# Kernel tuning notes

Measured on AMD Instinct MI355X. Metric: run time of the kernel, lower is better.

## Reference

```python
import jax, jax.numpy as jnp
import numpy as np
from jax import lax

SELECTION_SIZE = 2  # top-k experts per token


def setup_inputs() -> dict:
    key = jax.random.key(0)
    k1, k2, k3, k4 = jax.random.split(key, 4)
    N, E, IN, OUT = 8192, 8, 2048, 2048
    X = jax.random.normal(k1, (N, IN), dtype=jnp.float32)
    G = jax.random.normal(k2, (N, E), dtype=jnp.float32)
    # expert Linear params: y = x @ W_e.T + b_e, W_e: [out, in]
    W = jax.random.normal(k3, (E, OUT, IN), dtype=jnp.float32) * (1.0 / np.sqrt(IN))
    b = jax.random.normal(k4, (E, OUT), dtype=jnp.float32) * 0.01
    return {"X": X, "G": G, "W": W, "b": b}


def reference(X, G, W, b):
    # softmax gating over experts, then top-k selection and renormalization
    raw_weights = jax.nn.softmax(G, axis=1)                      # [N, E]
    top_w, top_idx = lax.top_k(raw_weights, SELECTION_SIZE)      # [N, k]
    norm_w = top_w / jnp.sum(top_w, axis=1, keepdims=True)       # [N, k]

    # dense all-expert GEMM (same math as per-expert gathered matmuls)
    all_Y = jnp.einsum('ni,eoi->neo', X, W) + b[None, :, :]      # [N, E, out]

    # gather the top-k experts' outputs per token and combine
    sel_Y = jnp.take_along_axis(all_Y, top_idx[:, :, None], axis=1)  # [N, k, out]
    Y = jnp.einsum('nk,nko->no', norm_w, sel_Y)                  # [N, out]
    return Y
```

## Files before the change

kernel.cpp:

```cpp
#include <hip/hip_runtime.h>
#include <hip/hip_bf16.h>

#define N_TOK 8192
#define N_EXP 8
#define DIM_IN 2048
#define DIM_OUT 2048

#define BM 256
#define BN 256
#define BK 64
#define NKT (DIM_IN / BK)

#define NX_ELEMS (N_TOK * DIM_IN)
#define NW_ELEMS (N_EXP * DIM_OUT * DIM_IN)

typedef __attribute__((ext_vector_type(8))) short bf16x8_t;
typedef __attribute__((ext_vector_type(8))) short s16x8_t;
typedef __attribute__((ext_vector_type(4))) short s16x4_t;
typedef __attribute__((ext_vector_type(4))) float f32x4_t;

__device__ __forceinline__ short f2bf(float f) {
    union { __hip_bfloat16 h; short s; } u;
    u.h = __float2bfloat16(f);
    return u.s;
}

__device__ __forceinline__ float bf2f(unsigned short s) {
    union { float f; unsigned u; } v;
    v.u = ((unsigned)s) << 16;
    return v.f;
}

__device__ __forceinline__ void gload_lds16(const void* g, void* l) {
    __builtin_amdgcn_global_load_lds(
        (const __attribute__((address_space(1))) void*)g,
        (__attribute__((address_space(3))) void*)l, 16, 0, 0);
}

__global__ void moe_zero_kernel(float4* __restrict__ y, int n4, int* __restrict__ counts) {
    int i = blockIdx.x * blockDim.x + threadIdx.x;
    if (i < N_EXP) counts[i] = 0;
    float4 z; z.x = 0.f; z.y = 0.f; z.z = 0.f; z.w = 0.f;
    for (; i < n4; i += gridDim.x * blockDim.x) y[i] = z;
}

__global__ void moe_cvt_kernel(const float* __restrict__ X, const float* __restrict__ W,
                               unsigned short* __restrict__ Xb, unsigned short* __restrict__ Wb,
                               const int* __restrict__ counts, int* __restrict__ base) {
    if (blockIdx.x == 0 && threadIdx.x == 0) {
        int s = 0;
#pragma unroll
        for (int e = 0; e < N_EXP; ++e) { base[e] = s; s += counts[e]; }
        base[N_EXP] = s;
    }
    const long long total8 = (long long)(NX_ELEMS + NW_ELEMS) / 8;
    for (long long i = blockIdx.x * blockDim.x + threadIdx.x; i < total8;
         i += (long long)gridDim.x * blockDim.x) {
        long long b8 = i * 8;
        const float* src;
        unsigned short* dst;
        if (b8 < NX_ELEMS) { src = X + b8; dst = Xb + b8; }
        else { src = W + (b8 - NX_ELEMS); dst = Wb + (b8 - NX_ELEMS); }
        f32x4_t a = __builtin_nontemporal_load((const f32x4_t*)src);
        f32x4_t b = __builtin_nontemporal_load((const f32x4_t*)(src + 4));
        s16x8_t h;
        h[0] = f2bf(a[0]); h[1] = f2bf(a[1]); h[2] = f2bf(a[2]); h[3] = f2bf(a[3]);
        h[4] = f2bf(b[0]); h[5] = f2bf(b[1]); h[6] = f2bf(b[2]); h[7] = f2bf(b[3]);
        *(s16x8_t*)dst = h;
    }
}

__global__ void moe_gate_kernel(const float* __restrict__ G,
                                int* __restrict__ counts,
                                int* __restrict__ lists,
                                float* __restrict__ lw,
                                int* __restrict__ slotA, int* __restrict__ slotB,
                                float* __restrict__ wAo, float* __restrict__ wBo) {
    int t = blockIdx.x * blockDim.x + threadIdx.x;
    if (t >= N_TOK) return;
    float g[N_EXP];
#pragma unroll
    for (int e = 0; e < N_EXP; ++e) g[e] = G[t * N_EXP + e];
    int i0 = 0; float b0 = g[0];
#pragma unroll
    for (int e = 1; e < N_EXP; ++e) if (g[e] > b0) { b0 = g[e]; i0 = e; }
    int i1 = -1; float b1 = -INFINITY;
#pragma unroll
    for (int e = 0; e < N_EXP; ++e) if (e != i0 && g[e] > b1) { b1 = g[e]; i1 = e; }
    float e1 = expf(b1 - b0);
    float w0 = 1.0f / (1.0f + e1);
    float w1 = e1 * w0;
    int p0 = atomicAdd(&counts[i0], 1);
    lists[i0 * N_TOK + p0] = t;
    lw[i0 * N_TOK + p0] = w0;
    int p1 = atomicAdd(&counts[i1], 1);
    lists[i1 * N_TOK + p1] = t;
    lw[i1 * N_TOK + p1] = w1;
    slotA[t] = (i0 << 13) | p0;
    slotB[t] = (i1 << 13) | p1;
    wAo[t] = w0;
    wBo[t] = w1;
}

__global__ __launch_bounds__(256) void moe_combine_kernel(
        const unsigned short* __restrict__ scratch, const int* __restrict__ base,
        const int* __restrict__ slotA, const int* __restrict__ slotB,
        const float* __restrict__ wA, const float* __restrict__ wB,
        float* __restrict__ Y) {
    const int t = blockIdx.x;
    const int c = threadIdx.x * 8;
    const int sa = slotA[t];
    const int sb = slotB[t];
    const long gA = base[sa >> 13] + (sa & 8191);
    const long gB = base[sb >> 13] + (sb & 8191);
    const float wa = wA[t], wb = wB[t];
    s16x8_t a = __builtin_nontemporal_load((const s16x8_t*)(scratch + gA * DIM_OUT + c));
    s16x8_t b = __builtin_nontemporal_load((const s16x8_t*)(scratch + gB * DIM_OUT + c));
    f32x4_t y0, y1;
#pragma unroll
    for (int j = 0; j < 4; ++j) {
        y0[j] = wa * bf2f((unsigned short)a[j])     + wb * bf2f((unsigned short)b[j]);
        y1[j] = wa * bf2f((unsigned short)a[j + 4]) + wb * bf2f((unsigned short)b[j + 4]);
    }
    f32x4_t* y = (f32x4_t*)(Y + (long)t * DIM_OUT + c);
    y[0] = y0;
    y[1] = y1;
}

__global__ __launch_bounds__(512, 2) void moe_gemm_bf16(
        const unsigned short* __restrict__ Xb, const unsigned short* __restrict__ Wb,
        const float* __restrict__ bias,
        const int* __restrict__ counts, const int* __restrict__ lists,
        const float* __restrict__ lw, const int* __restrict__ base,
        unsigned short* __restrict__ scratch, float* __restrict__ Y) {
    const int L = blockIdx.x + (DIM_OUT / BN) * (blockIdx.y + (N_TOK / BM) * blockIdx.z);
    const int e = L & 7;
    const int idx = L >> 3;
    const int M = counts[e];
    const int m0 = (idx >> 3) * BM;
    if (m0 >= M) return;
    int vr = M - m0; if (vr > BM) vr = BM;
    const int col0 = (idx & 7) * BN;

    __shared__ unsigned short As[2][BM * BK];
    __shared__ unsigned short Bs[2][BN * BK];

    const int tid = threadIdx.x;
    const int lane = tid & 63;
    const int wid = tid >> 6;
    const int wn = (wid & 3) * 64;

    const int* mylist = lists + e * N_TOK + m0;
    const float* lwp = lw + e * N_TOK + m0;

    const int srow = tid >> 3;
    const int scol = ((tid & 7) ^ (srow & 7)) * 8;

    const unsigned short* bptr = Wb + ((size_t)e * DIM_OUT + col0 + srow) * DIM_IN + scol;

    const int ldsbase = wid * 512;

    const int rl = lane & 15;
    const int hi = lane >> 4;
    const char* AsC = (const char*)As;
    const char* BsC = (const char*)Bs;

#define STAGE_B_H(buf, h, koff)                                                 \
    do {                                                                        \
        _Pragma("unroll")                                                       \
        for (int i = 2 * (h); i < 2 * (h) + 2; ++i)                             \
            gload_lds16(bptr + (size_t)(i * 64) * DIM_IN + (koff),              \
                        &Bs[buf][i * 4096 + ldsbase]);                          \
    } while (0)

    if (vr > 128) {
        const int wm = (wid >> 2) * 128;

        const unsigned short* aptr[4];
#pragma unroll
        for (int i = 0; i < 4; ++i) {
            int r = srow + 64 * i;
            int tok = (m0 + r < M) ? mylist[r] : mylist[0];
            aptr[i] = Xb + (size_t)tok * DIM_IN + scol;
        }

        unsigned vA[2], vB[2];
#pragma unroll
        for (int kk = 0; kk < 2; ++kk) {
            unsigned x = (unsigned)(((kk << 6) | (hi << 4)) ^ ((rl & 7) << 4));
            vA[kk] = (unsigned)((wm + rl) * 128) + x;
            vB[kk] = (unsigned)((wn + rl) * 128) + x;
        }

        f32x4_t acc[8][4];
#pragma unroll
        for (int m = 0; m < 8; ++m)
#pragma unroll
            for (int n = 0; n < 4; ++n)
                acc[m][n] = (f32x4_t)(0.0f);

#define STAGE_A_H(buf, h, koff)                                                 \
    do {                                                                        \
        _Pragma("unroll")                                                       \
        for (int i = 2 * (h); i < 2 * (h) + 2; ++i)                             \
            gload_lds16(aptr[i] + (koff), &As[buf][i * 4096 + ldsbase]);        \
    } while (0)

        STAGE_A_H(0, 0, 0);  STAGE_A_H(0, 1, 0);  STAGE_B_H(0, 0, 0);  STAGE_B_H(0, 1, 0);
        STAGE_A_H(1, 0, BK); STAGE_A_H(1, 1, BK); STAGE_B_H(1, 0, BK);

#define DO_TILE(CC, KOFN, KOF2)                                                 \
    {                                                                           \
        asm volatile("s_waitcnt vmcnt(6)" ::: "memory");                        \
        __builtin_amdgcn_s_barrier();                                           \
        asm volatile("" ::: "memory");                                          \
        STAGE_B_H(1 - (CC), 1, (KOFN));                                         \
        bf16x8_t bfr[4][2], af0[4][2], af1[4][2];                               \
        _Pragma("unroll")                                                       \
        for (int n = 0; n < 4; ++n)                                             \
            _Pragma("unroll")                                                   \
            for (int kk = 0; kk < 2; ++kk)                                      \
                bfr[n][kk] = *(const bf16x8_t*)(BsC + vB[kk] + ((CC) * 32768 + n * 2048)); \
        _Pragma("unroll")                                                       \
        for (int m = 0; m < 4; ++m)                                             \
            _Pragma("unroll")                                                   \
            for (int kk = 0; kk < 2; ++kk)                                      \
                af0[m][kk] = *(const bf16x8_t*)(AsC + vA[kk] + ((CC) * 32768 + m * 2048)); \
        __builtin_amdgcn_s_setprio(1);                                          \
        _Pragma("unroll")                                                       \
        for (int m = 0; m < 2; ++m)                                             \
            _Pragma("unroll")                                                   \
            for (int n = 0; n < 4; ++n)                                         \
                _Pragma("unroll")                                               \
                for (int kk = 0; kk < 2; ++kk)                                  \
                    acc[m][n] = __builtin_amdgcn_mfma_f32_16x16x32_bf16(af0[m][kk], bfr[n][kk], acc[m][n], 0, 0, 0); \
        __builtin_amdgcn_s_setprio(0);                                          \
        _Pragma("unroll")                                                       \
        for (int m = 0; m < 4; ++m)                                             \
            _Pragma("unroll")                                                   \
            for (int kk = 0; kk < 2; ++kk)                                      \
                af1[m][kk] = *(const bf16x8_t*)(AsC + vA[kk] + ((CC) * 32768 + (m + 4) * 2048)); \
        __builtin_amdgcn_s_setprio(1);                                          \
        _Pragma("unroll")                                                       \
        for (int m = 2; m < 4; ++m)                                             \
            _Pragma("unroll")                                                   \
            for (int n = 0; n < 4; ++n)                                         \
                _Pragma("unroll")                                               \
                for (int kk = 0; kk < 2; ++kk)                                  \
                    acc[m][n] = __builtin_amdgcn_mfma_f32_16x16x32_bf16(af0[m][kk], bfr[n][kk], acc[m][n], 0, 0, 0); \
        __builtin_amdgcn_s_setprio(0);                                          \
        asm volatile("s_waitcnt lgkmcnt(0)" ::: "memory");                      \
        __builtin_amdgcn_sched_barrier(0);                                      \
        __builtin_amdgcn_s_barrier();                                           \
        asm volatile("" ::: "memory");                                          \
        STAGE_A_H((CC), 0, (KOF2));                                             \
        __builtin_amdgcn_s_setprio(1);                                          \
        _Pragma("unroll")                                                       \
        for (int m = 0; m < 2; ++m)                                             \
            _Pragma("unroll")                                                   \
            for (int n = 0; n < 4; ++n)                                         \
                _Pragma("unroll")                                               \
                for (int kk = 0; kk < 2; ++kk)                                  \
                    acc[m + 4][n] = __builtin_amdgcn_mfma_f32_16x16x32_bf16(af1[m][kk], bfr[n][kk], acc[m + 4][n], 0, 0, 0); \
        __builtin_amdgcn_s_setprio(0);                                          \
        STAGE_A_H((CC), 1, (KOF2));                                             \
        __builtin_amdgcn_s_setprio(1);                                          \
        _Pragma("unroll")                                                       \
        for (int n = 0; n < 4; ++n)                                             \
            _Pragma("unroll")                                                   \
            for (int kk = 0; kk < 2; ++kk)                                      \
                acc[6][n] = __builtin_amdgcn_mfma_f32_16x16x32_bf16(af1[2][kk], bfr[n][kk], acc[6][n], 0, 0, 0); \
        __builtin_amdgcn_s_setprio(0);                                          \
        STAGE_B_H((CC), 0, (KOF2));                                             \
        __builtin_amdgcn_s_setprio(1);                                          \
        _Pragma("unroll")                                                       \
        for (int n = 0; n < 4; ++n)                                             \
            _Pragma("unroll")                                                   \
            for (int kk = 0; kk < 2; ++kk)                                      \
                acc[7][n] = __builtin_amdgcn_mfma_f32_16x16x32_bf16(af1[3][kk], bfr[n][kk], acc[7][n], 0, 0, 0); \
        __builtin_amdgcn_s_setprio(0);                                          \
    }

        for (int kt = 0; kt < NKT; kt += 2) {
            const int kofn0 = (kt + 1) * BK;
            const int kof20 = ((kt + 2 < NKT) ? (kt + 2) : (NKT - 1)) * BK;
            const int kofn1 = kof20;
            const int kof21 = ((kt + 3 < NKT) ? (kt + 3) : (NKT - 1)) * BK;
            DO_TILE(0, kofn0, kof20)
            DO_TILE(1, kofn1, kof21)
        }
        asm volatile("s_waitcnt vmcnt(0)" ::: "memory");

        const int cl = lane & 15;
        const int rq = (lane >> 4) << 2;
        float biasv[4];
#pragma unroll
        for (int n = 0; n < 4; ++n) biasv[n] = bias[e * DIM_OUT + col0 + wn + n * 16 + cl];

        if (scratch) {
            const int segbase = base[e] + m0;
#pragma unroll
            for (int m = 0; m < 8; ++m) {
#pragma unroll
                for (int j = 0; j < 4; ++j) {
                    int row = wm + (m << 4) + rq + j;
                    if (m0 + row < M) {
                        short* out = (short*)(scratch + (size_t)(segbase + row) * DIM_OUT + col0 + wn);
#pragma unroll
                        for (int n = 0; n < 4; ++n)
                            __builtin_nontemporal_store(f2bf(acc[m][n][j] + biasv[n]), out + n * 16 + cl);
                    }
                }
            }
        } else {
#pragma unroll
            for (int m = 0; m < 8; ++m) {
#pragma unroll
                for (int j = 0; j < 4; ++j) {
                    int row = wm + (m << 4) + rq + j;
                    if (m0 + row < M) {
                        int tok = mylist[row];
                        float wgt = lwp[row];
                        float* yrow = Y + (size_t)tok * DIM_OUT + col0 + wn;
#pragma unroll
                        for (int n = 0; n < 4; ++n)
                            atomicAdd(yrow + n * 16 + cl, wgt * (acc[m][n][j] + biasv[n]));
                    }
                }
            }
        }
    } else {
        const int wm = (wid >> 2) * 64;

        const unsigned short* aptrT[2];
#pragma unroll
        for (int i = 0; i < 2; ++i) {
            int r = srow + 64 * i;
            int tok = (m0 + r < M) ? mylist[r] : mylist[0];
            aptrT[i] = Xb + (size_t)tok * DIM_IN + scol;
        }

        unsigned vA[2], vB[2];
#pragma unroll
        for (int kk = 0; kk < 2; ++kk) {
            unsigned x = (unsigned)(((kk << 6) | (hi << 4)) ^ ((rl & 7) << 4));
            vA[kk] = (unsigned)((wm + rl) * 128) + x;
            vB[kk] = (unsigned)((wn + rl) * 128) + x;
        }

        f32x4_t acc[4][4];
#pragma unroll
        for (int m = 0; m < 4; ++m)
#pragma unroll
            for (int n = 0; n < 4; ++n)
                acc[m][n] = (f32x4_t)(0.0f);

#define STAGE_A_T(buf, koff)                                                    \
    do {                                                                        \
        _Pragma("unroll")                                                       \
        for (int i = 0; i < 2; ++i)                                             \
            gload_lds16(aptrT[i] + (koff), &As[buf][i * 4096 + ldsbase]);       \
    } while (0)

        STAGE_A_T(0, 0);  STAGE_B_H(0, 0, 0);  STAGE_B_H(0, 1, 0);
        STAGE_A_T(1, BK); STAGE_B_H(1, 0, BK);

#define DO_TILE_T(CC, KOFN, KOF2)                                               \
    {                                                                           \
        asm volatile("s_waitcnt vmcnt(4)" ::: "memory");                        \
        __builtin_amdgcn_s_barrier();                                           \
        asm volatile("" ::: "memory");                                          \
        STAGE_B_H(1 - (CC), 1, (KOFN));                                         \
        bf16x8_t bfr[4][2], af[4][2];                                           \
        _Pragma("unroll")                                                       \
        for (int n = 0; n < 4; ++n)                                             \
            _Pragma("unroll")                                                   \
            for (int kk = 0; kk < 2; ++kk)                                      \
                bfr[n][kk] = *(const bf16x8_t*)(BsC + vB[kk] + ((CC) * 32768 + n * 2048)); \
        _Pragma("unroll")                                                       \
        for (int m = 0; m < 4; ++m)                                             \
            _Pragma("unroll")                                                   \
            for (int kk = 0; kk < 2; ++kk)                                      \
                af[m][kk] = *(const bf16x8_t*)(AsC + vA[kk] + ((CC) * 32768 + m * 2048)); \
        __builtin_amdgcn_s_setprio(1);                                          \
        _Pragma("unroll")                                                       \
        for (int m = 0; m < 2; ++m)                                             \
            _Pragma("unroll")                                                   \
            for (int n = 0; n < 4; ++n)                                         \
                _Pragma("unroll")                                               \
                for (int kk = 0; kk < 2; ++kk)                                  \
                    acc[m][n] = __builtin_amdgcn_mfma_f32_16x16x32_bf16(af[m][kk], bfr[n][kk], acc[m][n], 0, 0, 0); \
        __builtin_amdgcn_s_setprio(0);                                          \
        asm volatile("s_waitcnt lgkmcnt(0)" ::: "memory");                      \
        __builtin_amdgcn_sched_barrier(0);                                      \
        __builtin_amdgcn_s_barrier();                                           \
        asm volatile("" ::: "memory");                                          \
        STAGE_A_T((CC), (KOF2));                                                \
        __builtin_amdgcn_s_setprio(1);                                          \
        _Pragma("unroll")                                                       \
        for (int m = 2; m < 4; ++m)                                             \
            _Pragma("unroll")                                                   \
            for (int n = 0; n < 4; ++n)                                         \
                _Pragma("unroll")                                               \
                for (int kk = 0; kk < 2; ++kk)                                  \
                    acc[m][n] = __builtin_amdgcn_mfma_f32_16x16x32_bf16(af[m][kk], bfr[n][kk], acc[m][n], 0, 0, 0); \
        __builtin_amdgcn_s_setprio(0);                                          \
        STAGE_B_H((CC), 0, (KOF2));                                             \
    }

        for (int kt = 0; kt < NKT; kt += 2) {
            const int kofn0 = (kt + 1) * BK;
            const int kof20 = ((kt + 2 < NKT) ? (kt + 2) : (NKT - 1)) * BK;
            const int kofn1 = kof20;
            const int kof21 = ((kt + 3 < NKT) ? (kt + 3) : (NKT - 1)) * BK;
            DO_TILE_T(0, kofn0, kof20)
            DO_TILE_T(1, kofn1, kof21)
        }
        asm volatile("s_waitcnt vmcnt(0)" ::: "memory");

        const int cl = lane & 15;
        const int rq = (lane >> 4) << 2;
        float biasv[4];
#pragma unroll
        for (int n = 0; n < 4; ++n) biasv[n] = bias[e * DIM_OUT + col0 + wn + n * 16 + cl];

        if (scratch) {
            const int segbase = base[e] + m0;
#pragma unroll
            for (int m = 0; m < 4; ++m) {
#pragma unroll
                for (int j = 0; j < 4; ++j) {
                    int row = wm + (m << 4) + rq + j;
                    if (m0 + row < M) {
                        short* out = (short*)(scratch + (size_t)(segbase + row) * DIM_OUT + col0 + wn);
#pragma unroll
                        for (int n = 0; n < 4; ++n)
                            __builtin_nontemporal_store(f2bf(acc[m][n][j] + biasv[n]), out + n * 16 + cl);
                    }
                }
            }
        } else {
#pragma unroll
            for (int m = 0; m < 4; ++m) {
#pragma unroll
                for (int j = 0; j < 4; ++j) {
                    int row = wm + (m << 4) + rq + j;
                    if (m0 + row < M) {
                        int tok = mylist[row];
                        float wgt = lwp[row];
                        float* yrow = Y + (size_t)tok * DIM_OUT + col0 + wn;
#pragma unroll
                        for (int n = 0; n < 4; ++n)
                            atomicAdd(yrow + n * 16 + cl, wgt * (acc[m][n][j] + biasv[n]));
                    }
                }
            }
        }
    }
#undef DO_TILE
#undef DO_TILE_T
#undef STAGE_A_H
#undef STAGE_A_T
#undef STAGE_B_H
}

__global__ __launch_bounds__(256, 2) void moe_gemm_f32(
        const float* __restrict__ X, const float* __restrict__ W,
        const float* __restrict__ bias,
        const int* __restrict__ counts, const int* __restrict__ lists,
        const float* __restrict__ lw, float* __restrict__ Y) {
    const int e = blockIdx.z;
    const int M = counts[e];
    const int m0 = blockIdx.y * 128;
    if (m0 >= M) return;
    const int col0 = blockIdx.x * 128;

    __shared__ short As[128 * 64];
    __shared__ short Bs[128 * 64];
    char* Ab = (char*)As;
    char* Bb = (char*)Bs;

    const int tid = threadIdx.x;
    const int lane = tid & 63;
    const int wid = tid >> 6;
    const int wm = (wid >> 1) * 64;
    const int wn = (wid & 1) * 64;

    const int* mylist = lists + e * N_TOK + m0;
    const float* lwp = lw + e * N_TOK + m0;

    const int srow = tid >> 4;
    const int scol = (tid & 15) << 2;
    const int swzW = (srow & 7) << 4;

    const float* xptr[8];
#pragma unroll
    for (int p = 0; p < 8; ++p) {
        int r = p * 16 + srow;
        int tok = (m0 + r < M) ? mylist[r] : mylist[0];
        xptr[p] = X + (size_t)tok * DIM_IN + scol;
    }
    const float* wptr = W + ((size_t)e * DIM_OUT + col0 + srow) * DIM_IN + scol;

    f32x4_t acc[4][4];
#pragma unroll
    for (int m = 0; m < 4; ++m)
#pragma unroll
        for (int n = 0; n < 4; ++n)
            acc[m][n] = (f32x4_t)(0.0f);

    for (int k0 = 0; k0 < DIM_IN; k0 += 64) {
#pragma unroll
        for (int p = 0; p < 8; ++p) {
            int r = p * 16 + srow;
            unsigned byteoff = (unsigned)(r * 128 + scol * 2) ^ swzW;
            float4 va = *(const float4*)(xptr[p] + k0);
            s16x4_t ha; ha[0] = f2bf(va.x); ha[1] = f2bf(va.y); ha[2] = f2bf(va.z); ha[3] = f2bf(va.w);
            *(s16x4_t*)(Ab + byteoff) = ha;
            float4 vb = *(const float4*)(wptr + (size_t)p * 16 * DIM_IN + k0);
            s16x4_t hb; hb[0] = f2bf(vb.x); hb[1] = f2bf(vb.y); hb[2] = f2bf(vb.z); hb[3] = f2bf(vb.w);
            *(s16x4_t*)(Bb + byteoff) = hb;
        }
        __syncthreads();

#pragma unroll
        for (int kk = 0; kk < 2; ++kk) {
            const int kb = (kk << 6) + ((lane >> 4) << 4);
            bf16x8_t af[4], bfr[4];
#pragma unroll
            for (int m = 0; m < 4; ++m) {
                int r = wm + (m << 4) + (lane & 15);
                unsigned byteoff = (unsigned)(r * 128 + kb) ^ ((unsigned)(r & 7) << 4);
                af[m] = *(const bf16x8_t*)(Ab + byteoff);
            }
#pragma unroll
            for (int n = 0; n < 4; ++n) {
                int r = wn + (n << 4) + (lane & 15);
                unsigned byteoff = (unsigned)(r * 128 + kb) ^ ((unsigned)(r & 7) << 4);
                bfr[n] = *(const bf16x8_t*)(Bb + byteoff);
            }
#pragma unroll
            for (int m = 0; m < 4; ++m)
#pragma unroll
                for (int n = 0; n < 4; ++n)
                    acc[m][n] = __builtin_amdgcn_mfma_f32_16x16x32_bf16(af[m], bfr[n], acc[m][n], 0, 0, 0);
        }
        __syncthreads();
    }

    const int cl = lane & 15;
    const int rq = (lane >> 4) << 2;
    float biasv[4];
#pragma unroll
    for (int n = 0; n < 4; ++n) biasv[n] = bias[e * DIM_OUT + col0 + wn + n * 16 + cl];
#pragma unroll
    for (int m = 0; m < 4; ++m) {
#pragma unroll
        for (int j = 0; j < 4; ++j) {
            int row = wm + (m << 4) + rq + j;
            if (m0 + row < M) {
                int tok = mylist[row];
                float wgt = lwp[row];
                float* yrow = Y + (size_t)tok * DIM_OUT + col0 + wn;
#pragma unroll
                for (int n = 0; n < 4; ++n)
                    atomicAdd(yrow + n * 16 + cl, wgt * (acc[m][n][j] + biasv[n]));
            }
        }
    }
}

extern "C" void kernel_launch(void* const* d_in, const int* in_sizes, int n_in,
                              void* d_out, int out_size, void* d_ws, size_t ws_size,
                              hipStream_t stream) {
    const float* X = (const float*)d_in[0];
    const float* G = (const float*)d_in[1];
    const float* W = (const float*)d_in[2];
    const float* b = (const float*)d_in[3];
    float* Y = (float*)d_out;

    char* ws = (char*)d_ws;
    int*   counts = (int*)ws;
    int*   base   = (int*)(ws + 64);
    int*   slotA  = (int*)(ws + 256);
    int*   slotB  = (int*)(ws + 256 + 32768);
    float* wA     = (float*)(ws + 256 + 65536);
    float* wB     = (float*)(ws + 256 + 98304);
    int*   lists  = (int*)(ws + 256 + 131072);
    float* lw     = (float*)(ws + 256 + 131072 + 262144);
    size_t o_Xb   = 256 + 131072 + 2 * 262144;
    unsigned short* Xb = (unsigned short*)(ws + o_Xb);
    size_t o_Wb   = o_Xb + (size_t)NX_ELEMS * 2;
    unsigned short* Wb = (unsigned short*)(ws + o_Wb);
    size_t o_scr  = o_Wb + (size_t)NW_ELEMS * 2;
    unsigned short* scratch = (unsigned short*)(ws + o_scr);
    const size_t ws_need_mid  = o_scr;
    const size_t ws_need_full = o_scr + (size_t)2 * N_TOK * DIM_OUT * 2;

    const bool use_scratch = (ws_size >= ws_need_full);
    const bool use_bf16    = (ws_size >= ws_need_mid);

    if (use_scratch) {
        moe_zero_kernel<<<1, 256, 0, stream>>>((float4*)Y, 0, counts);
    } else {
        moe_zero_kernel<<<2048, 256, 0, stream>>>((float4*)Y, out_size / 4, counts);
    }
    moe_gate_kernel<<<(N_TOK + 255) / 256, 256, 0, stream>>>(G, counts, lists, lw,
                                                             slotA, slotB, wA, wB);

    if (use_bf16) {
        moe_cvt_kernel<<<2048, 256, 0, stream>>>(X, W, Xb, Wb, counts, base);
        dim3 grid(DIM_OUT / BN, N_TOK / BM, N_EXP);
        moe_gemm_bf16<<<grid, 512, 0, stream>>>(Xb, Wb, b, counts, lists, lw, base,
                                                use_scratch ? scratch : nullptr, Y);
        if (use_scratch) {
            moe_combine_kernel<<<N_TOK, 256, 0, stream>>>(scratch, base, slotA, slotB,
                                                          wA, wB, Y);
        }
    } else {
        dim3 grid(DIM_OUT / 128, N_TOK / 128, N_EXP);
        moe_gemm_f32<<<grid, 256, 0, stream>>>(X, W, b, counts, lists, lw, Y);
    }
}
```

Baseline: 297.1 us.

## Restructure K-tile loop into four barrier-separated quadrant phases interleaving loads and MFMAs

Reorganizes each K-tile iteration into four phases (rows 0-3 × cols 0-1, rows 0-3 × cols 2-3, rows 4-7 × cols 0-1, rows 4-7 × cols 2-3). Each phase loads a partial set of LDS fragments, issues a slice of global->LDS prefetch, syncs with barriers, then runs MFMAs. The vmcnt wait and barrier move to the end of the tile, with one hoisted before the loop. The goal is a finer ping-pong schedule that overlaps LDS reads and global prefetch with MFMA work, at the cost of more barriers per tile. Correctness depends on the reordered buffer-overwrite timing still being safe.

```diff
diff --git a/kernel.cpp b/kernel.cpp
--- a/kernel.cpp
+++ b/kernel.cpp
@@ -208,16 +208,16 @@
 
         STAGE_A_H(0, 0, 0);  STAGE_A_H(0, 1, 0);  STAGE_B_H(0, 0, 0);  STAGE_B_H(0, 1, 0);
         STAGE_A_H(1, 0, BK); STAGE_A_H(1, 1, BK); STAGE_B_H(1, 0, BK);
+        asm volatile("s_waitcnt vmcnt(6)" ::: "memory");
+        __builtin_amdgcn_s_barrier();
+        asm volatile("" ::: "memory");
 
 #define DO_TILE(CC, KOFN, KOF2)                                                 \
     {                                                                           \
-        asm volatile("s_waitcnt vmcnt(6)" ::: "memory");                        \
-        __builtin_amdgcn_s_barrier();                                           \
-        asm volatile("" ::: "memory");                                          \
-        STAGE_B_H(1 - (CC), 1, (KOFN));                                         \
-        bf16x8_t bfr[4][2], af0[4][2], af1[4][2];                               \
-        _Pragma("unroll")                                                       \
-        for (int n = 0; n < 4; ++n)                                             \
+        bf16x8_t bfr[4][2], af03[4][2], af47[4][2];                             \
+         \
+        _Pragma("unroll")                                                       \
+        for (int n = 0; n < 2; ++n)                                             \
             _Pragma("unroll")                                                   \
             for (int kk = 0; kk < 2; ++kk)                                      \
                 bfr[n][kk] = *(const bf16x8_t*)(BsC + vB[kk] + ((CC) * 32768 + n * 2048)); \
@@ -225,60 +225,81 @@
         for (int m = 0; m < 4; ++m)                                             \
             _Pragma("unroll")                                                   \
             for (int kk = 0; kk < 2; ++kk)                                      \
-                af0[m][kk] = *(const bf16x8_t*)(AsC + vA[kk] + ((CC) * 32768 + m * 2048)); \
+                af03[m][kk] = *(const bf16x8_t*)(AsC + vA[kk] + ((CC) * 32768 + m * 2048)); \
+        STAGE_B_H(1 - (CC), 1, (KOFN));                                         \
+        __builtin_amdgcn_s_barrier();                                           \
+        asm volatile("" ::: "memory");                                          \
+        asm volatile("s_waitcnt lgkmcnt(0)" ::: "memory");                      \
+        __builtin_amdgcn_sched_barrier(0);                                      \
         __builtin_amdgcn_s_setprio(1);                                          \
         _Pragma("unroll")                                                       \
-        for (int m = 0; m < 2; ++m)                                             \
-            _Pragma("unroll")                                                   \
-            for (int n = 0; n < 4; ++n)                                         \
+        for (int m = 0; m < 4; ++m)                                             \
+            _Pragma("unroll")                                                   \
+            for (int n = 0; n < 2; ++n)                                         \
                 _Pragma("unroll")                                               \
                 for (int kk = 0; kk < 2; ++kk)                                  \
-                    acc[m][n] = __builtin_amdgcn_mfma_f32_16x16x32_bf16(af0[m][kk], bfr[n][kk], acc[m][n], 0, 0, 0); \
+                    acc[m][n] = __builtin_amdgcn_mfma_f32_16x16x32_bf16(af03[m][kk], bfr[n][kk], acc[m][n], 0, 0, 0); \
         __builtin_amdgcn_s_setprio(0);                                          \
+        __builtin_amdgcn_s_barrier();                                           \
+        asm volatile("" ::: "memory");                                          \
+                                  \
+        _Pragma("unroll")                                                       \
+        for (int n = 2; n < 4; ++n)                                             \
+            _Pragma("unroll")                                                   \
+            for (int kk = 0; kk < 2; ++kk)                                      \
+                bfr[n][kk] = *(const bf16x8_t*)(BsC + vB[kk] + ((CC) * 32768 + n * 2048)); \
+        __builtin_amdgcn_s_barrier();                                           \
+        asm volatile("" ::: "memory");                                          \
+        asm volatile("s_waitcnt lgkmcnt(0)" ::: "memory");                      \
+        __builtin_amdgcn_sched_barrier(0);                                      \
+        __builtin_amdgcn_s_setprio(1);                                          \
         _Pragma("unroll")                                                       \
         for (int m = 0; m < 4; ++m)                                             \
             _Pragma("unroll")                                                   \
-            for (int kk = 0; kk < 2; ++kk)                                      \
-                af1[m][kk] = *(const bf16x8_t*)(AsC + vA[kk] + ((CC) * 32768 + (m + 4) * 2048)); \
-        __builtin_amdgcn_s_setprio(1);                                          \
-        _Pragma("unroll")                                                       \
-        for (int m = 2; m < 4; ++m)                                             \
-            _Pragma("unroll")                                                   \
-            for (int n = 0; n < 4; ++n)                                         \
+            for (int n = 2; n < 4; ++n)                                         \
                 _Pragma("unroll")                                               \
                 for (int kk = 0; kk < 2; ++kk)                                  \
-                    acc[m][n] = __builtin_amdgcn_mfma_f32_16x16x32_bf16(af0[m][kk], bfr[n][kk], acc[m][n], 0, 0, 0); \
+                    acc[m][n] = __builtin_amdgcn_mfma_f32_16x16x32_bf16(af03[m][kk], bfr[n][kk], acc[m][n], 0, 0, 0); \
         __builtin_amdgcn_s_setprio(0);                                          \
+        __builtin_amdgcn_s_barrier();                                           \
+        asm volatile("" ::: "memory");                                          \
+              \
+        _Pragma("unroll")                                                       \
+        for (int m = 0; m < 4; ++m)                                             \
+            _Pragma("unroll")                                                   \
+            for (int kk = 0; kk < 2; ++kk)                                      \
+                af47[m][kk] = *(const bf16x8_t*)(AsC + vA[kk] + ((CC) * 32768 + (m + 4) * 2048)); \
+        STAGE_B_H((CC), 0, (KOF2));                                             \
+        __builtin_amdgcn_s_barrier();                                           \
+        asm volatile("" ::: "memory");                                          \
         asm volatile("s_waitcnt lgkmcnt(0)" ::: "memory");                      \
         __builtin_amdgcn_sched_barrier(0);                                      \
-        __builtin_amdgcn_s_barrier();                                           \
-        asm volatile("" ::: "memory");                                          \
-        STAGE_A_H((CC), 0, (KOF2));                                             \
         __builtin_amdgcn_s_setprio(1);                                          \
         _Pragma("unroll")                                                       \
-        for (int m = 0; m < 2; ++m)                                             \
-            _Pragma("unroll")                                                   \
-            for (int n = 0; n < 4; ++n)                                         \
+        for (int m = 0; m < 4; ++m)                                             \
+            _Pragma("unroll")                                                   \
+            for (int n = 0; n < 2; ++n)                                         \
                 _Pragma("unroll")                                               \
                 for (int kk = 0; kk < 2; ++kk)                                  \
-                    acc[m + 4][n] = __builtin_amdgcn_mfma_f32_16x16x32_bf16(af1[m][kk], bfr[n][kk], acc[m + 4][n], 0, 0, 0); \
+                    acc[m + 4][n] = __builtin_amdgcn_mfma_f32_16x16x32_bf16(af47[m][kk], bfr[n][kk], acc[m + 4][n], 0, 0, 0); \
         __builtin_amdgcn_s_setprio(0);                                          \
+        __builtin_amdgcn_s_barrier();                                           \
+        asm volatile("" ::: "memory");                                          \
+                \
+        STAGE_A_H((CC), 0, (KOF2));                                             \
         STAGE_A_H((CC), 1, (KOF2));                                             \
         __builtin_amdgcn_s_setprio(1);                                          \
         _Pragma("unroll")                                                       \
-        for (int n = 0; n < 4; ++n)                                             \
-            _Pragma("unroll")                                                   \
-            for (int kk = 0; kk < 2; ++kk)                                      \
-                acc[6][n] = __builtin_amdgcn_mfma_f32_16x16x32_bf16(af1[2][kk], bfr[n][kk], acc[6][n], 0, 0, 0); \
+        for (int m = 0; m < 4; ++m)                                             \
+            _Pragma("unroll")                                                   \
+            for (int n = 2; n < 4; ++n)                                         \
+                _Pragma("unroll")                                               \
+                for (int kk = 0; kk < 2; ++kk)                                  \
+                    acc[m + 4][n] = __builtin_amdgcn_mfma_f32_16x16x32_bf16(af47[m][kk], bfr[n][kk], acc[m + 4][n], 0, 0, 0); \
         __builtin_amdgcn_s_setprio(0);                                          \
-        STAGE_B_H((CC), 0, (KOF2));                                             \
-        __builtin_amdgcn_s_setprio(1);                                          \
-        _Pragma("unroll")                                                       \
-        for (int n = 0; n < 4; ++n)                                             \
-            _Pragma("unroll")                                                   \
-            for (int kk = 0; kk < 2; ++kk)                                      \
-                acc[7][n] = __builtin_amdgcn_mfma_f32_16x16x32_bf16(af1[3][kk], bfr[n][kk], acc[7][n], 0, 0, 0); \
-        __builtin_amdgcn_s_setprio(0);                                          \
+        asm volatile("s_waitcnt vmcnt(6)" ::: "memory");                        \
+        __builtin_amdgcn_s_barrier();                                           \
+        asm volatile("" ::: "memory");                                          \
     }
 
         for (int kt = 0; kt < NKT; kt += 2) {
```

Result: no change. 301.8 us (+1.6%).
